# Kernel tuning notes

Hardware: AMD Instinct MI355X
Metric: run time of the kernel (lower is better)

## Reference

```python
import jax, jax.numpy as jnp
import numpy as np

NEG_SLOPE = 0.2


def gat_layer(x, src, dst, W, attn_l, attn_r, bias):
    # x: [N, in_dim]; W: [in_dim, H*D]; attn_l/attn_r/bias: [H, D] / [H, D] / [H, D]
    N = x.shape[0]
    H, D = attn_l.shape
    feat = (x @ W).reshape(N, H, D)                      # [N, H, D]
    el = jnp.sum(feat * attn_l, axis=-1)                 # [N, H]
    er = jnp.sum(feat * attn_r, axis=-1)                 # [N, H]
    e = jax.nn.leaky_relu(el[src] + er[dst], NEG_SLOPE)  # [E, H]
    # edge softmax over incoming edges of each dst node (numerically stable)
    emax = jax.ops.segment_max(e, dst, num_segments=N)   # [N, H]
    ex = jnp.exp(e - emax[dst])                          # [E, H]
    denom = jax.ops.segment_sum(ex, dst, num_segments=N) # [N, H]
    alpha = ex / denom[dst]                              # [E, H]
    msg = alpha[:, :, None] * feat[src]                  # [E, H, D]
    rst = jax.ops.segment_sum(msg, dst, num_segments=N)  # [N, H, D]
    return rst + bias


def setup_inputs() -> dict:
    key = jax.random.key(0)
    ks = jax.random.split(key, 16)
    N, E = 50000, 800000
    IN, H, D, C = 128, 8, 16, 10
    HD = H * D  # 128
    s = lambda fan: 1.0 / np.sqrt(fan)
    return {
        "x": jax.random.normal(ks[0], (N, IN), jnp.float32),
        "src": jax.random.randint(ks[1], (E,), 0, N, jnp.int32),
        "dst": jax.random.randint(ks[2], (E,), 0, N, jnp.int32),
        "W1": jax.random.normal(ks[3], (IN, HD), jnp.float32) * s(IN),
        "al1": jax.random.normal(ks[4], (H, D), jnp.float32) * s(D),
        "ar1": jax.random.normal(ks[5], (H, D), jnp.float32) * s(D),
        "b1": jnp.zeros((H, D), jnp.float32),
        "W2": jax.random.normal(ks[6], (HD, HD), jnp.float32) * s(HD),
        "al2": jax.random.normal(ks[7], (H, D), jnp.float32) * s(D),
        "ar2": jax.random.normal(ks[8], (H, D), jnp.float32) * s(D),
        "b2": jnp.zeros((H, D), jnp.float32),
        "Wc": jax.random.normal(ks[9], (HD, C), jnp.float32) * s(HD),
        "bc": jnp.zeros((C,), jnp.float32),
    }


def reference(x, src, dst, W1, al1, ar1, b1, W2, al2, ar2, b2, Wc, bc):
    N = x.shape[0]
    h = gat_layer(x, src, dst, W1, al1, ar1, b1)       # [N, H, D]
    h = jax.nn.relu(h).reshape(N, -1)                  # [N, H*D]
    h = gat_layer(h, src, dst, W2, al2, ar2, b2)       # [N, H, D]
    hg = jnp.mean(h, axis=0).reshape(1, -1)            # mean_nodes, single graph -> [1, H*D]
    return hg @ Wc + bc                                # [1, num_classes]
```

## Files before the change

kernel.cpp:

```cpp
#include <hip/hip_runtime.h>
#include <hip/hip_bf16.h>

#define LEAKY 0.2f
#define BINB 8
#define TILE 4096
#define CAP 8192

static inline int ceil_div(int a, int b) { return (a + b - 1) / b; }

typedef __bf16 bf16x8 __attribute__((ext_vector_type(8)));
typedef float f32x4 __attribute__((ext_vector_type(4)));

__device__ __forceinline__ ushort f2bf(float f) {
    unsigned int x = __float_as_uint(f);
    unsigned int r = (x + 0x7fffu + ((x >> 16) & 1u)) >> 16;
    return (ushort)r;
}


__global__ __launch_bounds__(256) void bin_count(const int* __restrict__ dst,
                                                 int* __restrict__ bin_cnt, int E, int NB) {
    __shared__ int h[256];
    int t = threadIdx.x;
    h[t] = 0;
    __syncthreads();
    int base = blockIdx.x * TILE;
#pragma unroll
    for (int j = 0; j < TILE / 256; ++j) {
        int i = base + j * 256 + t;
        if (i < E) atomicAdd(&h[dst[i] >> BINB], 1);
    }
    __syncthreads();
    if (t < NB && h[t]) atomicAdd(&bin_cnt[t], h[t]);
}

__global__ __launch_bounds__(256) void bin_scan(const int* __restrict__ bin_cnt,
                                                int* __restrict__ binStart,
                                                int* __restrict__ bin_cursor,
                                                int* __restrict__ rowstart,
                                                int NB, int N, int E) {
    __shared__ int s[256];
    int t = threadIdx.x;
    int v = (t < NB) ? bin_cnt[t] : 0;
    s[t] = v;
    __syncthreads();
    for (int off = 1; off < 256; off <<= 1) {
        int x = (t >= off) ? s[t - off] : 0;
        __syncthreads();
        s[t] += x;
        __syncthreads();
    }
    int excl = s[t] - v;
    if (t < NB) {
        binStart[t] = excl;
        bin_cursor[t] = excl;
        if (t == NB - 1) binStart[NB] = excl + v;
    }
    if (t == 0) rowstart[N] = E;
}

__global__ __launch_bounds__(256) void bin_scatter(const int* __restrict__ src,
                                                   const int* __restrict__ dst,
                                                   int* __restrict__ bin_cursor,
                                                   unsigned int* __restrict__ coarse, int E) {
    __shared__ int hist[256], scn[256], gbase[256], lcur[256];
    __shared__ unsigned int outp[TILE];
    __shared__ int gidx[TILE];
    int t = threadIdx.x;
    hist[t] = 0;
    __syncthreads();
    int base = blockIdx.x * TILE;
    int dloc[TILE / 256];
#pragma unroll
    for (int j = 0; j < TILE / 256; ++j) {
        int i = base + j * 256 + t;
        int d = (i < E) ? dst[i] : -1;
        dloc[j] = d;
        if (d >= 0) atomicAdd(&hist[d >> BINB], 1);
    }
    __syncthreads();
    int hv = hist[t];
    scn[t] = hv;
    __syncthreads();
    for (int off = 1; off < 256; off <<= 1) {
        int x = (t >= off) ? scn[t - off] : 0;
        __syncthreads();
        scn[t] += x;
        __syncthreads();
    }
    int excl = scn[t] - hv;
    if (hv > 0) gbase[t] = atomicAdd(&bin_cursor[t], hv);
    lcur[t] = excl;
    scn[t] = excl;
    __syncthreads();
#pragma unroll
    for (int j = 0; j < TILE / 256; ++j) {
        int i = base + j * 256 + t;
        int d = dloc[j];
        if (d >= 0) {
            int b = d >> BINB;
            int pos = atomicAdd(&lcur[b], 1);
            outp[pos] = (unsigned int)src[i] | ((unsigned int)(d & ((1 << BINB) - 1)) << 16);
            gidx[pos] = gbase[b] + (pos - scn[b]);
        }
    }
    __syncthreads();
    int cnt = min(TILE, E - base);
    for (int j = t; j < cnt; j += 256) coarse[gidx[j]] = outp[j];
}

__global__ __launch_bounds__(256) void fine_csr(const unsigned int* __restrict__ coarse,
                                                const int* __restrict__ binStart,
                                                int* __restrict__ rowstart,
                                                ushort* __restrict__ bucket, int N) {
    __shared__ int hist[256], scn[256], cur[256];
    __shared__ ushort sb[CAP];
    int b = blockIdx.x, t = threadIdx.x;
    int e0 = binStart[b], e1 = binStart[b + 1];
    int cnt = e1 - e0;
    hist[t] = 0;
    __syncthreads();
    for (int j = e0 + t; j < e1; j += 256) atomicAdd(&hist[coarse[j] >> 16], 1);
    __syncthreads();
    int hv = hist[t];
    scn[t] = hv;
    __syncthreads();
    for (int off = 1; off < 256; off <<= 1) {
        int x = (t >= off) ? scn[t - off] : 0;
        __syncthreads();
        scn[t] += x;
        __syncthreads();
    }
    int excl = scn[t] - hv;
    int n = (b << BINB) + t;
    if (n < N) rowstart[n] = e0 + excl;
    cur[t] = excl;
    __syncthreads();
    bool fit = (cnt <= CAP);
    for (int j = e0 + t; j < e1; j += 256) {
        unsigned int p = coarse[j];
        int dl = p >> 16;
        int pos = atomicAdd(&cur[dl], 1);
        ushort sv = (ushort)(p & 0xffffu);
        if (fit) sb[pos] = sv;
        else bucket[e0 + pos] = sv;
    }
    __syncthreads();
    if (fit)
        for (int j = t; j < cnt; j += 256) bucket[e0 + j] = sb[j];
}

__global__ __launch_bounds__(256) void convert_w(const float* __restrict__ W1,
                                                 const float* __restrict__ W2,
                                                 ushort* __restrict__ Wt1,
                                                 ushort* __restrict__ Wt2) {
    int idx = blockIdx.x * 256 + threadIdx.x;
    const float* W = (idx < 16384) ? W1 : W2;
    ushort* O = (idx < 16384) ? Wt1 : Wt2;
    int i = idx & 16383;
    int k = i >> 7, n = i & 127;
    O[n * 128 + k] = f2bf(W[i]);
}

#define LDK 136
__global__ __launch_bounds__(256) void gemm_attn_mfma(const float* __restrict__ in,
                                                      const ushort* __restrict__ Wt,
                                                      const float* __restrict__ al,
                                                      const float* __restrict__ ar,
                                                      ushort* __restrict__ feat,
                                                      float* __restrict__ el,
                                                      float* __restrict__ er, int N) {
    __shared__ ushort sA[64 * LDK];
    int tid = threadIdx.x;
    int rowbase = blockIdx.x * 64;

#pragma unroll
    for (int i = 0; i < 8; ++i) {
        int idx4 = i * 256 + tid;
        int flat = idx4 * 4;
        int row = flat >> 7, col = flat & 127;
        int grow = rowbase + row;
        float4 v = make_float4(0.f, 0.f, 0.f, 0.f);
        if (grow < N) v = *reinterpret_cast<const float4*>(in + (size_t)grow * 128 + col);
        uint2 w;
        w.x = (unsigned int)f2bf(v.x) | ((unsigned int)f2bf(v.y) << 16);
        w.y = (unsigned int)f2bf(v.z) | ((unsigned int)f2bf(v.w) << 16);
        *reinterpret_cast<uint2*>(&sA[row * LDK + col]) = w;
    }
    __syncthreads();

    int wid = tid >> 6;
    int lane = tid & 63;
    int wm = wid >> 1;
    int wn = wid & 1;
    int l15 = lane & 15;
    int lhi = lane >> 4;

    f32x4 acc[2][4] = {};
    const ushort* wb = Wt + (size_t)(wn * 64 + l15) * 128 + lhi * 8;
    const ushort* a0p = &sA[(wm * 32 + l15) * LDK + lhi * 8];
    const ushort* a1p = &sA[(wm * 32 + 16 + l15) * LDK + lhi * 8];

#pragma unroll
    for (int ks = 0; ks < 4; ++ks) {
        bf16x8 a0 = *reinterpret_cast<const bf16x8*>(a0p + ks * 32);
        bf16x8 a1 = *reinterpret_cast<const bf16x8*>(a1p + ks * 32);
#pragma unroll
        for (int ni = 0; ni < 4; ++ni) {
            bf16x8 b = *reinterpret_cast<const bf16x8*>(wb + ni * 16 * 128 + ks * 32);
            acc[0][ni] = __builtin_amdgcn_mfma_f32_16x16x32_bf16(a0, b, acc[0][ni], 0, 0, 0);
            acc[1][ni] = __builtin_amdgcn_mfma_f32_16x16x32_bf16(a1, b, acc[1][ni], 0, 0, 0);
        }
    }

#pragma unroll
    for (int ni = 0; ni < 4; ++ni) {
        int head = wn * 4 + ni;
        float alv = al[head * 16 + l15];
        float arv = ar[head * 16 + l15];
#pragma unroll
        for (int mi = 0; mi < 2; ++mi) {
#pragma unroll
            for (int reg = 0; reg < 4; ++reg) {
                int row = rowbase + wm * 32 + mi * 16 + lhi * 4 + reg;
                float v = acc[mi][ni][reg];
                float pl = v * alv;
                float pr = v * arv;
#pragma unroll
                for (int off = 8; off; off >>= 1) {
                    pl += __shfl_xor(pl, off);
                    pr += __shfl_xor(pr, off);
                }
                if (row < N) {
                    feat[(size_t)row * 128 + head * 16 + l15] = f2bf(v);
                    if (l15 == 0) {
                        el[row * 8 + head] = pl;
                        er[row * 8 + head] = pr;
                    }
                }
            }
        }
    }
}

__global__ __launch_bounds__(256) void aggregate(const ushort* __restrict__ feat,
                                                 const float* __restrict__ el,
                                                 const float* __restrict__ er,
                                                 const int* __restrict__ rowstart,
                                                 const ushort* __restrict__ bucket,
                                                 const float* __restrict__ bias,
                                                 float* __restrict__ out,
                                                 int N, int do_relu) {
    int wid = (blockIdx.x * 256 + threadIdx.x) >> 6;
    int lane = threadIdx.x & 63;
    if (wid >= N) return;
    int h = lane >> 3;
    float er_h = er[wid * 8 + h];
    int beg = rowstart[wid];
    int end = rowstart[wid + 1];

    const unsigned int* fp = reinterpret_cast<const unsigned int*>(feat) + lane;

    float l = 0.0f, ax = 0.0f, ay = 0.0f;

    for (int base = beg; base < end; base += 64) {
        int cnt = min(end - base, 64);
        int myedge = base + lane;
        int sv = (myedge < end) ? (int)bucket[myedge] : 0;
        int k = 0;
        for (; k + 8 <= cnt; k += 8) {
            int ss[8];
            float ee[8];
            unsigned int uu[8];
#pragma unroll
            for (int q = 0; q < 8; ++q) ss[q] = __shfl(sv, k + q);
#pragma unroll
            for (int q = 0; q < 8; ++q) ee[q] = el[ss[q] * 8 + h];
#pragma unroll
            for (int q = 0; q < 8; ++q) uu[q] = fp[ss[q] * 64];
#pragma unroll
            for (int q = 0; q < 8; ++q) {
                float e = ee[q] + er_h;
                e = (e > 0.0f) ? e : LEAKY * e;
                float p = __expf(e);
                l += p;
                ax = fmaf(p, __uint_as_float(uu[q] << 16), ax);
                ay = fmaf(p, __uint_as_float(uu[q] & 0xffff0000u), ay);
            }
        }
        for (; k < cnt; ++k) {
            int s = __shfl(sv, k);
            float e = el[s * 8 + h] + er_h;
            e = (e > 0.0f) ? e : LEAKY * e;
            float p = __expf(e);
            unsigned int u = fp[s * 64];
            l += p;
            ax = fmaf(p, __uint_as_float(u << 16), ax);
            ay = fmaf(p, __uint_as_float(u & 0xffff0000u), ay);
        }
    }

    float inv = (end > beg) ? 1.0f / l : 0.0f;
    int c = lane * 2;
    float2 bv = *reinterpret_cast<const float2*>(bias + c);
    float ox = fmaf(ax, inv, bv.x);
    float oy = fmaf(ay, inv, bv.y);
    if (do_relu) {
        ox = fmaxf(ox, 0.0f);
        oy = fmaxf(oy, 0.0f);
    }
    float2 o = {ox, oy};
    *reinterpret_cast<float2*>(out + (size_t)wid * 128 + c) = o;
}

__global__ __launch_bounds__(256) void mean_reduce(const float* __restrict__ h,
                                                   float* __restrict__ meanbuf, int N) {
    int c = threadIdx.x & 127;
    int rbase = blockIdx.x * 2 + (threadIdx.x >> 7);
    float s = 0.0f;
    for (int r = rbase; r < N; r += gridDim.x * 2) s += h[r * 128 + c];
    atomicAdd(&meanbuf[c], s);
}

__global__ __launch_bounds__(64) void classifier(const float* __restrict__ meanbuf,
                                                 const float* __restrict__ Wc,
                                                 const float* __restrict__ bc,
                                                 float* __restrict__ outp, float invN) {
    int j = threadIdx.x;
    if (j < 10) {
        float s = 0.0f;
        for (int k = 0; k < 128; ++k) s += meanbuf[k] * invN * Wc[k * 10 + j];
        outp[j] = s + bc[j];
    }
}


extern "C" void kernel_launch(void* const* d_in, const int* in_sizes, int n_in,
                              void* d_out, int out_size, void* d_ws, size_t ws_size,
                              hipStream_t stream) {
    const float* x   = (const float*)d_in[0];
    const int*   src = (const int*)d_in[1];
    const int*   dst = (const int*)d_in[2];
    const float* W1  = (const float*)d_in[3];
    const float* al1 = (const float*)d_in[4];
    const float* ar1 = (const float*)d_in[5];
    const float* b1  = (const float*)d_in[6];
    const float* W2  = (const float*)d_in[7];
    const float* al2 = (const float*)d_in[8];
    const float* ar2 = (const float*)d_in[9];
    const float* b2  = (const float*)d_in[10];
    const float* Wc  = (const float*)d_in[11];
    const float* bc  = (const float*)d_in[12];

    int N = in_sizes[0] / 128;
    int E = in_sizes[1];
    int NB = (N + (1 << BINB) - 1) >> BINB;

    size_t off = 0;
    auto alloc = [&](size_t bytes) -> void* {
        void* p = (char*)d_ws + off;
        off += (bytes + 255) & ~size_t(255);
        return p;
    };
    int*   bin_cnt    = (int*)alloc(sizeof(int) * NB);
    int*   binStart   = (int*)alloc(sizeof(int) * (NB + 1));
    int*   bin_cursor = (int*)alloc(sizeof(int) * NB);
    int*   rowstart   = (int*)alloc(sizeof(int) * (N + 1));
    unsigned int* coarse = (unsigned int*)alloc(sizeof(unsigned int) * E);
    ushort* bucket  = (ushort*)alloc(sizeof(ushort) * E);
    ushort* feat    = (ushort*)alloc(sizeof(ushort) * (size_t)N * 128);
    float* el       = (float*)alloc(sizeof(float) * N * 8);
    float* er       = (float*)alloc(sizeof(float) * N * 8);
    float* h1       = (float*)alloc(sizeof(float) * (size_t)N * 128);
    float* h2       = (float*)alloc(sizeof(float) * (size_t)N * 128);
    float* meanbuf  = (float*)alloc(sizeof(float) * 128);
    ushort* Wt1     = (ushort*)alloc(sizeof(ushort) * 128 * 128);
    ushort* Wt2     = (ushort*)alloc(sizeof(ushort) * 128 * 128);

    hipMemsetAsync(bin_cnt, 0, sizeof(int) * NB, stream);
    hipMemsetAsync(meanbuf, 0, sizeof(float) * 128, stream);

    int GB = ceil_div(E, TILE);

    bin_count<<<GB, 256, 0, stream>>>(dst, bin_cnt, E, NB);
    bin_scan<<<1, 256, 0, stream>>>(bin_cnt, binStart, bin_cursor, rowstart, NB, N, E);
    bin_scatter<<<GB, 256, 0, stream>>>(src, dst, bin_cursor, coarse, E);
    fine_csr<<<NB, 256, 0, stream>>>(coarse, binStart, rowstart, bucket, N);
    convert_w<<<128, 256, 0, stream>>>(W1, W2, Wt1, Wt2);

    gemm_attn_mfma<<<ceil_div(N, 64), 256, 0, stream>>>(x, Wt1, al1, ar1, feat, el, er, N);
    aggregate<<<ceil_div(N * 64, 256), 256, 0, stream>>>(feat, el, er, rowstart, bucket, b1, h1, N, 1);
    gemm_attn_mfma<<<ceil_div(N, 64), 256, 0, stream>>>(h1, Wt2, al2, ar2, feat, el, er, N);
    aggregate<<<ceil_div(N * 64, 256), 256, 0, stream>>>(feat, el, er, rowstart, bucket, b2, h2, N, 0);
    mean_reduce<<<256, 256, 0, stream>>>(h2, meanbuf, N);
    classifier<<<1, 64, 0, stream>>>(meanbuf, Wc, bc, (float*)d_out, 1.0f / (float)N);
}
```

Baseline: 216.7 us.

## Store hidden activations in bf16 and compute edge logits once per edge-head

Intermediate hidden layers h1/h2 are now written as bf16 instead of fp32. The second GEMM reads bf16 directly without converting, and mean_reduce reads bf16, which roughly halves the traffic for those buffers. The aggregate kernel is also restructured so each lane computes one (edge, head) attention logit and exp, shared through shuffles, instead of every lane redoing the el load and exp for all 8 edges. This removes redundant gathers and transcendentals but adds shuffles and a final cross-lane reduction of the denominator, and it adds bf16 rounding of the activations.

```diff
diff --git a/kernel.cpp b/kernel.cpp
--- a/kernel.cpp
+++ b/kernel.cpp
@@ -163,7 +163,8 @@
 }
 
 #define LDK 136
-__global__ __launch_bounds__(256) void gemm_attn_mfma(const float* __restrict__ in,
+template <bool BF16IN>
+__global__ __launch_bounds__(256) void gemm_attn_mfma(const void* __restrict__ in_,
                                                       const ushort* __restrict__ Wt,
                                                       const float* __restrict__ al,
                                                       const float* __restrict__ ar,
@@ -174,18 +175,33 @@
     int tid = threadIdx.x;
     int rowbase = blockIdx.x * 64;
 
-#pragma unroll
-    for (int i = 0; i < 8; ++i) {
-        int idx4 = i * 256 + tid;
-        int flat = idx4 * 4;
-        int row = flat >> 7, col = flat & 127;
-        int grow = rowbase + row;
-        float4 v = make_float4(0.f, 0.f, 0.f, 0.f);
-        if (grow < N) v = *reinterpret_cast<const float4*>(in + (size_t)grow * 128 + col);
-        uint2 w;
-        w.x = (unsigned int)f2bf(v.x) | ((unsigned int)f2bf(v.y) << 16);
-        w.y = (unsigned int)f2bf(v.z) | ((unsigned int)f2bf(v.w) << 16);
-        *reinterpret_cast<uint2*>(&sA[row * LDK + col]) = w;
+    if (BF16IN) {
+        const ushort* in = (const ushort*)in_;
+#pragma unroll
+        for (int i = 0; i < 4; ++i) {
+            int idx8 = i * 256 + tid;
+            int flat = idx8 * 8;
+            int row = flat >> 7, col = flat & 127;
+            int grow = rowbase + row;
+            uint4 v = make_uint4(0, 0, 0, 0);
+            if (grow < N) v = *reinterpret_cast<const uint4*>(in + (size_t)grow * 128 + col);
+            *reinterpret_cast<uint4*>(&sA[row * LDK + col]) = v;
+        }
+    } else {
+        const float* in = (const float*)in_;
+#pragma unroll
+        for (int i = 0; i < 8; ++i) {
+            int idx4 = i * 256 + tid;
+            int flat = idx4 * 4;
+            int row = flat >> 7, col = flat & 127;
+            int grow = rowbase + row;
+            float4 v = make_float4(0.f, 0.f, 0.f, 0.f);
+            if (grow < N) v = *reinterpret_cast<const float4*>(in + (size_t)grow * 128 + col);
+            uint2 w;
+            w.x = (unsigned int)f2bf(v.x) | ((unsigned int)f2bf(v.y) << 16);
+            w.y = (unsigned int)f2bf(v.z) | ((unsigned int)f2bf(v.w) << 16);
+            *reinterpret_cast<uint2*>(&sA[row * LDK + col]) = w;
+        }
     }
     __syncthreads();
 
@@ -249,58 +265,68 @@
                                                  const int* __restrict__ rowstart,
                                                  const ushort* __restrict__ bucket,
                                                  const float* __restrict__ bias,
-                                                 float* __restrict__ out,
+                                                 ushort* __restrict__ out,
                                                  int N, int do_relu) {
     int wid = (blockIdx.x * 256 + threadIdx.x) >> 6;
     int lane = threadIdx.x & 63;
     if (wid >= N) return;
-    int h = lane >> 3;
-    float er_h = er[wid * 8 + h];
+    int l7 = lane & 7;
+    int e8 = lane >> 3;
+    float erv = er[wid * 8 + l7];
     int beg = rowstart[wid];
     int end = rowstart[wid + 1];
 
     const unsigned int* fp = reinterpret_cast<const unsigned int*>(feat) + lane;
 
-    float l = 0.0f, ax = 0.0f, ay = 0.0f;
+    float lsum = 0.0f, ax = 0.0f, ay = 0.0f;
 
     for (int base = beg; base < end; base += 64) {
         int cnt = min(end - base, 64);
         int myedge = base + lane;
-        int sv = (myedge < end) ? (int)bucket[myedge] : 0;
+        int sv64 = ((myedge < end) ? (int)bucket[myedge] : 0) << 6;
+
         int k = 0;
         for (; k + 8 <= cnt; k += 8) {
-            int ss[8];
-            float ee[8];
-            unsigned int uu[8];
-#pragma unroll
-            for (int q = 0; q < 8; ++q) ss[q] = __shfl(sv, k + q);
-#pragma unroll
-            for (int q = 0; q < 8; ++q) ee[q] = el[ss[q] * 8 + h];
-#pragma unroll
-            for (int q = 0; q < 8; ++q) uu[q] = fp[ss[q] * 64];
-#pragma unroll
-            for (int q = 0; q < 8; ++q) {
-                float e = ee[q] + er_h;
-                e = (e > 0.0f) ? e : LEAKY * e;
-                float p = __expf(e);
-                l += p;
-                ax = fmaf(p, __uint_as_float(uu[q] << 16), ax);
-                ay = fmaf(p, __uint_as_float(uu[q] & 0xffff0000u), ay);
-            }
-        }
-        for (; k < cnt; ++k) {
-            int s = __shfl(sv, k);
-            float e = el[s * 8 + h] + er_h;
+            int se = __shfl(sv64, k + e8);
+            float e = el[(se >> 3) + l7] + erv;
             e = (e > 0.0f) ? e : LEAKY * e;
             float p = __expf(e);
-            unsigned int u = fp[s * 64];
-            l += p;
-            ax = fmaf(p, __uint_as_float(u << 16), ax);
-            ay = fmaf(p, __uint_as_float(u & 0xffff0000u), ay);
-        }
-    }
-
-    float inv = (end > beg) ? 1.0f / l : 0.0f;
+            lsum += p;
+#pragma unroll
+            for (int q = 0; q < 8; ++q) {
+                int su = __shfl(sv64, k + q);
+                float pq = __shfl(p, q * 8 + e8);
+                unsigned int u = fp[su];
+                ax = fmaf(pq, __uint_as_float(u << 16), ax);
+                ay = fmaf(pq, __uint_as_float(u & 0xffff0000u), ay);
+            }
+        }
+        if (k < cnt) {
+            int se = __shfl(sv64, min(k + e8, cnt - 1));
+            bool valid = (k + e8) < cnt;
+            float e = el[(se >> 3) + l7] + erv;
+            e = (e > 0.0f) ? e : LEAKY * e;
+            float p = valid ? __expf(e) : 0.0f;
+            lsum += p;
+#pragma unroll
+            for (int q = 0; q < 8; ++q) {
+                if (k + q < cnt) {
+                    int su = __shfl(sv64, k + q);
+                    float pq = __shfl(p, q * 8 + e8);
+                    unsigned int u = fp[su];
+                    ax = fmaf(pq, __uint_as_float(u << 16), ax);
+                    ay = fmaf(pq, __uint_as_float(u & 0xffff0000u), ay);
+                }
+            }
+        }
+    }
+
+    lsum += __shfl_xor(lsum, 8);
+    lsum += __shfl_xor(lsum, 16);
+    lsum += __shfl_xor(lsum, 32);
+    float denom = __shfl(lsum, e8);
+    float inv = (end > beg) ? 1.0f / denom : 0.0f;
+
     int c = lane * 2;
     float2 bv = *reinterpret_cast<const float2*>(bias + c);
     float ox = fmaf(ax, inv, bv.x);
@@ -309,16 +335,17 @@
         ox = fmaxf(ox, 0.0f);
         oy = fmaxf(oy, 0.0f);
     }
-    float2 o = {ox, oy};
-    *reinterpret_cast<float2*>(out + (size_t)wid * 128 + c) = o;
-}
-
-__global__ __launch_bounds__(256) void mean_reduce(const float* __restrict__ h,
+    unsigned int pk = (unsigned int)f2bf(ox) | ((unsigned int)f2bf(oy) << 16);
+    reinterpret_cast<unsigned int*>(out)[(size_t)wid * 64 + lane] = pk;
+}
+
+__global__ __launch_bounds__(256) void mean_reduce(const ushort* __restrict__ h,
                                                    float* __restrict__ meanbuf, int N) {
     int c = threadIdx.x & 127;
     int rbase = blockIdx.x * 2 + (threadIdx.x >> 7);
     float s = 0.0f;
-    for (int r = rbase; r < N; r += gridDim.x * 2) s += h[r * 128 + c];
+    for (int r = rbase; r < N; r += gridDim.x * 2)
+        s += __uint_as_float((unsigned int)h[(size_t)r * 128 + c] << 16);
     atomicAdd(&meanbuf[c], s);
 }
 
@@ -371,8 +398,8 @@
     ushort* feat    = (ushort*)alloc(sizeof(ushort) * (size_t)N * 128);
     float* el       = (float*)alloc(sizeof(float) * N * 8);
     float* er       = (float*)alloc(sizeof(float) * N * 8);
-    float* h1       = (float*)alloc(sizeof(float) * (size_t)N * 128);
-    float* h2       = (float*)alloc(sizeof(float) * (size_t)N * 128);
+    ushort* h1      = (ushort*)alloc(sizeof(ushort) * (size_t)N * 128);
+    ushort* h2      = (ushort*)alloc(sizeof(ushort) * (size_t)N * 128);
     float* meanbuf  = (float*)alloc(sizeof(float) * 128);
     ushort* Wt1     = (ushort*)alloc(sizeof(ushort) * 128 * 128);
     ushort* Wt2     = (ushort*)alloc(sizeof(ushort) * 128 * 128);
@@ -388,9 +415,9 @@
     fine_csr<<<NB, 256, 0, stream>>>(coarse, binStart, rowstart, bucket, N);
     convert_w<<<128, 256, 0, stream>>>(W1, W2, Wt1, Wt2);
 
-    gemm_attn_mfma<<<ceil_div(N, 64), 256, 0, stream>>>(x, Wt1, al1, ar1, feat, el, er, N);
+    gemm_attn_mfma<false><<<ceil_div(N, 64), 256, 0, stream>>>(x, Wt1, al1, ar1, feat, el, er, N);
     aggregate<<<ceil_div(N * 64, 256), 256, 0, stream>>>(feat, el, er, rowstart, bucket, b1, h1, N, 1);
-    gemm_attn_mfma<<<ceil_div(N, 64), 256, 0, stream>>>(h1, Wt2, al2, ar2, feat, el, er, N);
+    gemm_attn_mfma<true><<<ceil_div(N, 64), 256, 0, stream>>>(h1, Wt2, al2, ar2, feat, el, er, N);
     aggregate<<<ceil_div(N * 64, 256), 256, 0, stream>>>(feat, el, er, rowstart, bucket, b2, h2, N, 0);
     mean_reduce<<<256, 256, 0, stream>>>(h2, meanbuf, N);
     classifier<<<1, 64, 0, stream>>>(meanbuf, Wc, bc, (float*)d_out, 1.0f / (float)N);
```

After: 214.4 us. Within noise of the previous version (-1.1%).
